# Performance work log

Measured on AMD Instinct MI355X. Metric: run time of the kernel, lower is better.

## Reference

```python
import jax, jax.numpy as jnp
import numpy as np
from jax import lax

B, ROWS, COLS, K, LATENT = 8, 1536, 16, 32, 16
EPS_REG = 0.01  # torchsort regularization_strength
BIG = 1e30


def setup_inputs() -> dict:
    key = jax.random.key(0)
    ks = jax.random.split(key, 12)
    def w(k, shape):
        return (jax.random.normal(k, shape, jnp.float32) / np.sqrt(shape[0])).astype(jnp.float32)
    return {
        "table": jax.random.uniform(ks[0], (B, ROWS, COLS), jnp.float32),
        "enc_w1": w(ks[1], (COLS, 32)), "enc_b1": 0.01 * jax.random.normal(ks[2], (32,), jnp.float32),
        "enc_w2": w(ks[3], (32, 64)),   "enc_b2": 0.01 * jax.random.normal(ks[4], (64,), jnp.float32),
        "mean_w": w(ks[5], (64, LATENT)), "mean_b": 0.01 * jax.random.normal(ks[6], (LATENT,), jnp.float32),
        "dec_w1": w(ks[7], (LATENT, 32)), "dec_b1": 0.01 * jax.random.normal(ks[8], (32,), jnp.float32),
        "dec_w2": w(ks[9], (32, COLS)),   "dec_b2": 0.01 * jax.random.normal(ks[10], (COLS,), jnp.float32),
        "labels": jax.random.randint(ks[11], (ROWS,), 0, K, jnp.int32),
        "BlockSize": 64,
        "current_epoch": 0,
        "baseline": 0,
    }


def _soft_rank_l2(s, eps):
    # Exact soft_rank (Blondel et al. / torchsort, l2 reg, ascending):
    # project s/eps onto permutahedron of (n,...,1).
    n = s.shape[0]
    x = s / eps
    perm = jnp.argsort(-x)            # descending sort
    xs = x[perm]
    w = jnp.arange(n, 0, -1, dtype=x.dtype)
    # dual = non-increasing isotonic fit of y = xs - w == -iso_inc(-(xs - w))
    y = -(xs - w)
    S = jnp.concatenate([jnp.zeros((1,), x.dtype), jnp.cumsum(y)])
    idx = jnp.arange(n)
    length = jnp.maximum(idx[None, :] - idx[:, None] + 1, 1).astype(x.dtype)
    A = (S[1:][None, :] - S[:n][:, None]) / length           # mean(y[j..k])  [j,k]
    A = jnp.where(idx[None, :] >= idx[:, None], A, BIG)
    Bm = lax.cummin(A, axis=1, reverse=True)                  # min_{k>=i} A[j,k]
    Cm = lax.cummax(Bm, axis=0)                               # max_{j<=i} ...
    iso_inc = jnp.diagonal(Cm)
    dual = -iso_inc
    primal = xs - dual
    inv = jnp.argsort(perm)
    return primal[inv]


def _forward(table, enc_w1, enc_b1, enc_w2, enc_b2, mean_w, mean_b,
             dec_w1, dec_b1, dec_w2, dec_b2, labels, BlockSize):
    b = table.shape[0]
    # VAE (autoencoder path; z = latent mean)
    h = jax.nn.relu(table @ enc_w1 + enc_b1)
    h = jax.nn.relu(h @ enc_w2 + enc_b2)
    z = h @ mean_w + mean_b                                   # [B, rows, 16]
    r = jax.nn.relu(z @ dec_w1 + dec_b1)
    recon = jax.nn.relu(r @ dec_w2 + dec_b2)
    loss = jnp.mean((recon - table) ** 2)
    # clustering scores (labels fixed from batch 0, shared across batch)
    onehot = jax.nn.one_hot(labels, K, dtype=z.dtype)         # [rows, K]
    counts = jnp.maximum(onehot.sum(0), 1.0)                  # [K]
    centers = jnp.einsum('brd,rk->bkd', z, onehot) / counts[None, :, None]
    center_data = centers[:, labels, :]                       # gather back [B, rows, 16]
    d2 = jnp.mean((z - center_data) ** 2, axis=-1)            # [B, rows]
    mn = d2.min(axis=1, keepdims=True); mx = d2.max(axis=1, keepdims=True)
    d2 = (d2 - mn) / (mx - mn)
    scores = d2 + labels.astype(z.dtype)[None, :]
    # training branch
    smn = scores.min(axis=1, keepdims=True); smx = scores.max(axis=1, keepdims=True)
    scaled = (scores - smn) / (smx - smn) * jnp.asarray(b, z.dtype)  # * len(table)
    ranks = jax.vmap(lambda s: _soft_rank_l2(s, EPS_REG))(scaled)
    rank_idx = jnp.argsort(jnp.argsort(scores, axis=1), axis=1) // BlockSize + 1
    rows = table.shape[1]
    return (ranks.reshape(b, rows, 1), rank_idx.reshape(b, rows, 1),
            scores.reshape(b, rows, 1), loss)


def reference(table, enc_w1, enc_b1, enc_w2, enc_b2, mean_w, mean_b,
              dec_w1, dec_b1, dec_w2, dec_b2, labels, BlockSize,
              current_epoch, baseline):
    return _forward(table, enc_w1, enc_b1, enc_w2, enc_b2, mean_w, mean_b,
                    dec_w1, dec_b1, dec_w2, dec_b2, labels, BlockSize)
```

## Files before the change

kernel.cpp:

```cpp
#include <hip/hip_runtime.h>

#define BATCH 8
#define ROWS 1536
#define KCLS 32
#define NTOT (BATCH*ROWS)
#define ELEMS (NTOT*16)
#define SSTRIDE 3073
#define BIGF 1.0e30f

enum : int {
  WS_Z     = 0,
  WS_X     = WS_Z + NTOT*16,
  WS_XS    = WS_X + NTOT,
  WS_S     = WS_XS + NTOT,
  WS_DESC  = WS_S + BATCH*SSTRIDE,
  WS_ASCP  = WS_DESC + NTOT,
  WS_DSCP  = WS_ASCP + 4*NTOT,
  WS_GPART = WS_DSCP + 4*NTOT,
  WS_LOSSP = WS_GPART + BATCH*96*512,
};
#define WS_CPART WS_GPART

#define LW1  0
#define LB1  512
#define LW2  544
#define LB2  2592
#define LMW  2656
#define LMB  3680
#define LDW1 3696
#define LDB1 4208
#define LDW2 4240
#define LDB2 4752
#define LTOT 4768

#define AX   0
#define AH1  16
#define AH2  48
#define AZ   112
#define AR1  128
#define AREC 144
#define ASTRIDE 164

#define RPB 16

template<int IN_BASE, int IN_N, int OUT_BASE, int OUT_PW, int OUT_TOT,
         int WOFF, int BOFF, bool RELU>
__device__ __forceinline__ void layerw(float* __restrict__ act,
                                       const float* __restrict__ wsh,
                                       int lrow, int fway)
{
  const int o0 = fway * OUT_PW;
  float acc[OUT_PW];
#pragma unroll
  for (int j = 0; j < OUT_PW; ++j) acc[j] = wsh[BOFF + o0 + j];

  const float4* arow = reinterpret_cast<const float4*>(&act[lrow*ASTRIDE + IN_BASE]);
#pragma unroll 2
  for (int i4 = 0; i4 < IN_N/4; ++i4) {
    float4 sv = arow[i4];
    float svx[4];
    svx[0] = sv.x; svx[1] = sv.y; svx[2] = sv.z; svx[3] = sv.w;
#pragma unroll
    for (int u = 0; u < 4; ++u) {
      const float s = svx[u];
      const float* wp = &wsh[WOFF + (i4*4 + u)*OUT_TOT + o0];
      if constexpr (OUT_PW == 1) {
        acc[0] = fmaf(s, wp[0], acc[0]);
      } else if constexpr (OUT_PW == 2) {
        float2 w = *reinterpret_cast<const float2*>(wp);
        acc[0] = fmaf(s, w.x, acc[0]);
        acc[1] = fmaf(s, w.y, acc[1]);
      } else {
#pragma unroll
        for (int q = 0; q < OUT_PW/4; ++q) {
          float4 w = reinterpret_cast<const float4*>(wp)[q];
          acc[q*4+0] = fmaf(s, w.x, acc[q*4+0]);
          acc[q*4+1] = fmaf(s, w.y, acc[q*4+1]);
          acc[q*4+2] = fmaf(s, w.z, acc[q*4+2]);
          acc[q*4+3] = fmaf(s, w.w, acc[q*4+3]);
        }
      }
    }
  }
  float* orow = &act[lrow*ASTRIDE + OUT_BASE + o0];
  if constexpr (OUT_PW == 1) {
    orow[0] = RELU ? fmaxf(acc[0], 0.f) : acc[0];
  } else if constexpr (OUT_PW == 2) {
    float2 v;
    v.x = RELU ? fmaxf(acc[0], 0.f) : acc[0];
    v.y = RELU ? fmaxf(acc[1], 0.f) : acc[1];
    *reinterpret_cast<float2*>(orow) = v;
  } else {
#pragma unroll
    for (int q = 0; q < OUT_PW/4; ++q) {
      float4 v;
      v.x = RELU ? fmaxf(acc[q*4+0], 0.f) : acc[q*4+0];
      v.y = RELU ? fmaxf(acc[q*4+1], 0.f) : acc[q*4+1];
      v.z = RELU ? fmaxf(acc[q*4+2], 0.f) : acc[q*4+2];
      v.w = RELU ? fmaxf(acc[q*4+3], 0.f) : acc[q*4+3];
      reinterpret_cast<float4*>(orow)[q] = v;
    }
  }
}

__global__ __launch_bounds__(256, 4) void k1_ae(
    const float* __restrict__ table,
    const float* __restrict__ w1, const float* __restrict__ b1,
    const float* __restrict__ w2, const float* __restrict__ b2,
    const float* __restrict__ mw, const float* __restrict__ mb,
    const float* __restrict__ dw1, const float* __restrict__ db1,
    const float* __restrict__ dw2, const float* __restrict__ db2,
    const int* __restrict__ labels,
    float* __restrict__ ws)
{
  const int tid  = threadIdx.x;
  const int lrow = tid & (RPB-1);
  const int fway = tid >> 4;
  const int blk  = blockIdx.x;
  const int b    = blk / 96;
  const int ch   = blk % 96;

  __shared__ float wsh[LTOT];
  __shared__ float act[RPB * ASTRIDE];
  __shared__ int   lbl[RPB];
  __shared__ float lred[4];

  {
    float4* d4 = reinterpret_cast<float4*>(wsh);
#define CPY(off, src, nf4) \
    { const float4* p = reinterpret_cast<const float4*>(src); \
      for (int t = tid; t < (nf4); t += 256) d4[(off)/4 + t] = p[t]; }
    CPY(LW1,  w1,  128) CPY(LB1,  b1,  8)  CPY(LW2,  w2,  512)
    CPY(LB2,  b2,  16)  CPY(LMW,  mw,  256) CPY(LMB,  mb,  4)
    CPY(LDW1, dw1, 128) CPY(LDB1, db1, 8)  CPY(LDW2, dw2, 128)
    CPY(LDB2, db2, 4)
#undef CPY
    if (tid < RPB) lbl[tid] = labels[ch * RPB + tid];
    if (tid < RPB*4) {
      const float4 v = reinterpret_cast<const float4*>(table)[blk*(RPB*4) + tid];
      reinterpret_cast<float4*>(act)[(tid >> 2)*(ASTRIDE/4) + (tid & 3)] = v;
    }
  }
  __syncthreads();

  layerw<AX,  16, AH1, 2, 32, LW1,  LB1,  true >(act, wsh, lrow, fway);
  __syncthreads();
  layerw<AH1, 32, AH2, 4, 64, LW2,  LB2,  true >(act, wsh, lrow, fway);
  __syncthreads();
  layerw<AH2, 64, AZ,  1, 16, LMW,  LMB,  false>(act, wsh, lrow, fway);
  __syncthreads();

  if (tid < RPB*4) {
    const float4 zv =
      reinterpret_cast<const float4*>(act)[(tid >> 2)*(ASTRIDE/4) + (AZ/4) + (tid & 3)];
    reinterpret_cast<float4*>(ws + WS_Z)[blk*(RPB*4) + tid] = zv;
  }

  layerw<AZ,  16, AR1, 2, 32, LDW1, LDB1, true >(act, wsh, lrow, fway);
  __syncthreads();
  layerw<AR1, 32, AREC,1, 16, LDW2, LDB2, true >(act, wsh, lrow, fway);
  __syncthreads();

  {
    const float d = act[lrow*ASTRIDE + AREC + fway] - act[lrow*ASTRIDE + AX + fway];
    float ls = d * d;
    for (int off = 32; off > 0; off >>= 1) ls += __shfl_down(ls, off);
    if ((tid & 63) == 0) lred[tid >> 6] = ls;
    __syncthreads();
    if (tid == 0) ws[WS_LOSSP + blk] = (lred[0] + lred[1]) + (lred[2] + lred[3]);
  }

  {
    float a0 = 0.f, a1 = 0.f;
    const int d0 = tid & 15, k0 = tid >> 4;
    const int k1c = k0 + 16;
#pragma unroll
    for (int rr = 0; rr < RPB; ++rr) {
      const int lb = lbl[rr];
      const float zv = act[rr*ASTRIDE + AZ + d0];
      a0 += (lb == k0)  ? zv : 0.f;
      a1 += (lb == k1c) ? zv : 0.f;
    }
    ws[WS_CPART + (b*96 + ch)*512 + tid]       = a0;
    ws[WS_CPART + (b*96 + ch)*512 + 256 + tid] = a1;
  }
}

__global__ __launch_bounds__(256) void kmid(const int* __restrict__ labels,
                                            float* __restrict__ ws,
                                            float* __restrict__ out)
{
  const int bi = blockIdx.x;
  const int jb = bi & 3, rb = (bi >> 2) % 6, b = bi / 24;
  const int tid = threadIdx.x;

  __shared__ int   cnt[KCLS];
  __shared__ int   lbl_l[ROWS];
  __shared__ float cent[512];
  alignas(16) __shared__ float s_l[ROWS];
  alignas(16) __shared__ float d2x[ROWS];
  __shared__ float rmn[256], rmx[256];

  if (tid < KCLS) cnt[tid] = 0;
  if (bi == 0) {
    rmn[tid] = ws[WS_LOSSP + tid] + ws[WS_LOSSP + 256 + tid] + ws[WS_LOSSP + 512 + tid];
  }
  __syncthreads();
#pragma unroll
  for (int c = 0; c < 6; ++c) {
    const int lb = labels[c*256 + tid];
    lbl_l[c*256 + tid] = lb;
    atomicAdd(&cnt[lb], 1);
  }
  if (bi == 0) {
    for (int off = 128; off > 0; off >>= 1) {
      __syncthreads();
      if (tid < off) rmn[tid] += rmn[tid + off];
    }
    if (tid == 0) out[3*NTOT] = rmn[0] / (float)ELEMS;
  }
  __syncthreads();

#pragma unroll
  for (int e = tid; e < 512; e += 256) {
    float s = 0.f;
    for (int c = 0; c < 96; ++c) s += ws[WS_CPART + (b*96 + c)*512 + e];
    const int cn = cnt[e >> 4] > 1 ? cnt[e >> 4] : 1;
    cent[e] = s / (float)cn;
  }
  __syncthreads();

  float tmn = 3.0e38f, tmx = -3.0e38f;
#pragma unroll
  for (int c = 0; c < 6; ++c) {
    const int r = c*256 + tid;
    const int lb = lbl_l[r];
    const float4* zp = reinterpret_cast<const float4*>(ws + WS_Z + (b*ROWS + r)*16);
    const float4* cp = reinterpret_cast<const float4*>(&cent[lb*16]);
    float s = 0.f;
#pragma unroll
    for (int q = 0; q < 4; ++q) {
      float4 zv = zp[q], cv = cp[q];
      float d0 = zv.x - cv.x, d1 = zv.y - cv.y, d2_ = zv.z - cv.z, d3 = zv.w - cv.w;
      s += d0*d0 + d1*d1 + d2_*d2_ + d3*d3;
    }
    const float dv = s / 16.f;
    d2x[r] = dv;
    tmn = fminf(tmn, dv); tmx = fmaxf(tmx, dv);
  }
  rmn[tid] = tmn; rmx[tid] = tmx;
  __syncthreads();
  for (int off = 128; off > 0; off >>= 1) {
    if (tid < off) {
      rmn[tid] = fminf(rmn[tid], rmn[tid + off]);
      rmx[tid] = fmaxf(rmx[tid], rmx[tid + off]);
    }
    __syncthreads();
  }
  const float mn = rmn[0], mx = rmx[0];
  __syncthreads();

  tmn = 3.0e38f; tmx = -3.0e38f;
#pragma unroll
  for (int c = 0; c < 6; ++c) {
    const int r = c*256 + tid;
    const float sc = (d2x[r] - mn) / (mx - mn) + (float)lbl_l[r];
    s_l[r] = sc;
    if (jb == 0 && c == rb) out[2*NTOT + b*ROWS + r] = sc;
    tmn = fminf(tmn, sc); tmx = fmaxf(tmx, sc);
  }
  rmn[tid] = tmn; rmx[tid] = tmx;
  __syncthreads();
  for (int off = 128; off > 0; off >>= 1) {
    if (tid < off) {
      rmn[tid] = fminf(rmn[tid], rmn[tid + off]);
      rmx[tid] = fmaxf(rmx[tid], rmx[tid + off]);
    }
    __syncthreads();
  }
  const float smn = rmn[0], smx = rmx[0];
  __syncthreads();

#pragma unroll
  for (int c = 0; c < 6; ++c) {
    const int r = c*256 + tid;
    const float scl = (s_l[r] - smn) / (smx - smn) * 8.0f;
    const float xv = scl / 0.01f;
    d2x[r] = xv;
    if (jb == 0 && c == rb) ws[WS_X + b*ROWS + r] = xv;
  }
  __syncthreads();

  const int r0 = rb*256 + tid;
  const float si = s_l[r0], xi = d2x[r0];
  int asc = 0, dsc = 0;
  const int j0 = jb*384;
  const float4* s4p = reinterpret_cast<const float4*>(&s_l[j0]);
  const float4* x4p = reinterpret_cast<const float4*>(&d2x[j0]);
#pragma unroll 4
  for (int kk = 0; kk < 96; ++kk) {
    const float4 s4 = s4p[kk];
    const float4 x4 = x4p[kk];
    const int j = j0 + kk*4;
    asc += (s4.x < si || (s4.x == si && j   < r0)) ? 1 : 0;
    asc += (s4.y < si || (s4.y == si && j+1 < r0)) ? 1 : 0;
    asc += (s4.z < si || (s4.z == si && j+2 < r0)) ? 1 : 0;
    asc += (s4.w < si || (s4.w == si && j+3 < r0)) ? 1 : 0;
    dsc += (x4.x > xi || (x4.x == xi && j   < r0)) ? 1 : 0;
    dsc += (x4.y > xi || (x4.y == xi && j+1 < r0)) ? 1 : 0;
    dsc += (x4.z > xi || (x4.z == xi && j+2 < r0)) ? 1 : 0;
    dsc += (x4.w > xi || (x4.w == xi && j+3 < r0)) ? 1 : 0;
  }
  int* wsi = reinterpret_cast<int*>(ws);
  wsi[WS_ASCP + jb*NTOT + b*ROWS + r0] = asc;
  wsi[WS_DSCP + jb*NTOT + b*ROWS + r0] = dsc;
}

__global__ __launch_bounds__(256) void k67(const int* __restrict__ bsp,
                                           float* __restrict__ ws,
                                           float* __restrict__ out)
{
  const int b = blockIdx.x, tid = threadIdx.x;
  const int lane = tid & 63, wav = tid >> 6;
  __shared__ float xs_l[ROWS];
  __shared__ float wtot[4];
  const int* wsi = reinterpret_cast<const int*>(ws);
  int* wsw = reinterpret_cast<int*>(ws);
  const int BS = *bsp;
#pragma unroll
  for (int c = 0; c < 6; ++c) {
    const int r = c*256 + tid;
    const int idx = b*ROWS + r;
    int asc = 0, dsc = 0;
#pragma unroll
    for (int jb = 0; jb < 4; ++jb) {
      asc += wsi[WS_ASCP + jb*NTOT + idx];
      dsc += wsi[WS_DSCP + jb*NTOT + idx];
    }
    out[NTOT + idx] = (float)(asc / BS + 1);
    wsw[WS_DESC + idx] = dsc;
    xs_l[dsc] = ws[WS_X + idx];
  }
  __syncthreads();
  const int base = tid * 6;
  float y[6], own = 0.f;
#pragma unroll
  for (int u = 0; u < 6; ++u) {
    ws[WS_XS + b*ROWS + base + u] = xs_l[base + u];
    y[u] = (float)(ROWS - (base + u)) - xs_l[base + u];
    own += y[u];
  }
  float v = own;
#pragma unroll
  for (int d = 1; d < 64; d <<= 1) {
    float o = __shfl_up(v, d);
    if (lane >= d) v += o;
  }
  if (lane == 63) wtot[wav] = v;
  __syncthreads();
  float wpre = 0.f;
  for (int w = 0; w < wav; ++w) wpre += wtot[w];
  float run = wpre + (v - own);
  float* S = ws + WS_S + b*SSTRIDE;
#pragma unroll
  for (int u = 0; u < 6; ++u) { S[base + u] = run; run += y[u]; }
  if (tid == 255) S[ROWS] = run;
#pragma unroll
  for (int u = 0; u < 6; ++u) S[ROWS + 1 + tid*6 + u] = BIGF;
}

__global__ __launch_bounds__(256) void k8a(float* __restrict__ ws)
{
  const int bi = blockIdx.x;
  const int c = bi & 7, ib = (bi >> 3) % 6, b = bi / 48;
  const int tid = threadIdx.x;
  __shared__ float Sseg[448];
  __shared__ float invl[192];
  const float* S = ws + WS_S + b*SSTRIDE;
  const int ibase = ib*256;
  const int segbase = ibase + c*192 + 1;
  Sseg[tid] = S[segbase + tid];
  if (tid < 192) {
    Sseg[256 + tid] = S[segbase + 256 + tid];
    invl[tid] = 1.0f / (float)(c*192 + tid + 1);
  }
  __syncthreads();
  const int i = ibase + tid;
  const float Si = S[i];
  float gm = 3.0e38f;
#pragma unroll 8
  for (int k = 0; k < 192; ++k)
    gm = fminf(gm, (Sseg[tid + k] - Si) * invl[k]);
  ws[WS_GPART + (b*8 + c)*ROWS + i] = gm;
}

__global__ __launch_bounds__(768) void k8b(float* __restrict__ ws,
                                           float* __restrict__ out)
{
  const int b = blockIdx.x, tid = threadIdx.x;
  const int lane = tid & 63, wav = tid >> 6;
  __shared__ float g[ROWS];
  __shared__ float wtot[12];
  for (int t = tid; t < ROWS; t += 768) {
    float gm = 3.0e38f;
#pragma unroll
    for (int c = 0; c < 8; ++c)
      gm = fminf(gm, ws[WS_GPART + (b*8 + c)*ROWS + t]);
    g[t] = gm;
  }
  __syncthreads();
  const float a = g[2*tid], cc = g[2*tid + 1];
  float v = fmaxf(a, cc);
#pragma unroll
  for (int d = 1; d < 64; d <<= 1) {
    float o = __shfl_up(v, d);
    if (lane >= d) v = fmaxf(v, o);
  }
  if (lane == 63) wtot[wav] = v;
  __syncthreads();
  float wpre = -3.0e38f;
  for (int w = 0; w < wav; ++w) wpre = fmaxf(wpre, wtot[w]);
  float lex = __shfl_up(v, 1);
  if (lane == 0) lex = -3.0e38f;
  const float excl = fmaxf(wpre, lex);
  const float i0 = fmaxf(excl, a);
  const float i1 = fmaxf(i0, cc);
  g[2*tid] = i0; g[2*tid + 1] = i1;
  __syncthreads();
  const float* xs = ws + WS_XS + b*ROWS;
  const int* desc = reinterpret_cast<const int*>(ws) + WS_DESC + b*ROWS;
  for (int t = tid; t < ROWS; t += 768) {
    const int dr = desc[t];
    out[b*ROWS + t] = xs[dr] + g[dr];
  }
}

extern "C" void kernel_launch(void* const* d_in, const int* in_sizes, int n_in,
                              void* d_out, int out_size, void* d_ws, size_t ws_size,
                              hipStream_t stream) {
  const float* table = (const float*)d_in[0];
  const float* w1  = (const float*)d_in[1];
  const float* b1  = (const float*)d_in[2];
  const float* w2  = (const float*)d_in[3];
  const float* b2  = (const float*)d_in[4];
  const float* mw  = (const float*)d_in[5];
  const float* mb  = (const float*)d_in[6];
  const float* dw1 = (const float*)d_in[7];
  const float* db1 = (const float*)d_in[8];
  const float* dw2 = (const float*)d_in[9];
  const float* db2 = (const float*)d_in[10];
  const int* labels = (const int*)d_in[11];
  const int* bsp    = (const int*)d_in[12];
  float* out = (float*)d_out;
  float* ws  = (float*)d_ws;

  k1_ae<<<768, 256, 0, stream>>>(table, w1, b1, w2, b2, mw, mb, dw1, db1, dw2, db2, labels, ws);
  kmid<<<192, 256, 0, stream>>>(labels, ws, out);
  k67<<<8, 256, 0, stream>>>(bsp, ws, out);
  k8a<<<384, 256, 0, stream>>>(ws);
  k8b<<<8, 768, 0, stream>>>(ws, out);
}
```

Baseline: 66.00 us.

## Split kmid into centroid/distance kernel and counting kernel to avoid redundant work

```diff
diff --git a/kernel.cpp b/kernel.cpp
--- a/kernel.cpp
+++ b/kernel.cpp
@@ -18,6 +18,8 @@
   WS_DSCP  = WS_ASCP + 4*NTOT,
   WS_GPART = WS_DSCP + 4*NTOT,
   WS_LOSSP = WS_GPART + BATCH*96*512,
+  WS_D2    = WS_LOSSP + 768,
+  WS_MM    = WS_D2 + NTOT,
 };
 #define WS_CPART WS_GPART
 
@@ -186,55 +188,42 @@
   }
 }
 
-__global__ __launch_bounds__(256) void kmid(const int* __restrict__ labels,
+__global__ __launch_bounds__(256) void kcd2(const int* __restrict__ labels,
                                             float* __restrict__ ws,
                                             float* __restrict__ out)
 {
   const int bi = blockIdx.x;
-  const int jb = bi & 3, rb = (bi >> 2) % 6, b = bi / 24;
+  const int b = bi / 6, ib = bi % 6;
   const int tid = threadIdx.x;
 
   __shared__ int   cnt[KCLS];
-  __shared__ int   lbl_l[ROWS];
+  __shared__ int   lbls[256];
   __shared__ float cent[512];
-  alignas(16) __shared__ float s_l[ROWS];
-  alignas(16) __shared__ float d2x[ROWS];
   __shared__ float rmn[256], rmx[256];
 
   if (tid < KCLS) cnt[tid] = 0;
-  if (bi == 0) {
-    rmn[tid] = ws[WS_LOSSP + tid] + ws[WS_LOSSP + 256 + tid] + ws[WS_LOSSP + 512 + tid];
-  }
   __syncthreads();
 #pragma unroll
   for (int c = 0; c < 6; ++c) {
     const int lb = labels[c*256 + tid];
-    lbl_l[c*256 + tid] = lb;
+    if (c == ib) lbls[tid] = lb;
     atomicAdd(&cnt[lb], 1);
-  }
-  if (bi == 0) {
-    for (int off = 128; off > 0; off >>= 1) {
-      __syncthreads();
-      if (tid < off) rmn[tid] += rmn[tid + off];
-    }
-    if (tid == 0) out[3*NTOT] = rmn[0] / (float)ELEMS;
   }
   __syncthreads();
 
 #pragma unroll
   for (int e = tid; e < 512; e += 256) {
     float s = 0.f;
+#pragma unroll 8
     for (int c = 0; c < 96; ++c) s += ws[WS_CPART + (b*96 + c)*512 + e];
     const int cn = cnt[e >> 4] > 1 ? cnt[e >> 4] : 1;
     cent[e] = s / (float)cn;
   }
   __syncthreads();
 
-  float tmn = 3.0e38f, tmx = -3.0e38f;
-#pragma unroll
-  for (int c = 0; c < 6; ++c) {
-    const int r = c*256 + tid;
-    const int lb = lbl_l[r];
+  const int r = ib*256 + tid;
+  {
+    const int lb = lbls[tid];
     const float4* zp = reinterpret_cast<const float4*>(ws + WS_Z + (b*ROWS + r)*16);
     const float4* cp = reinterpret_cast<const float4*>(&cent[lb*16]);
     float s = 0.f;
@@ -245,10 +234,9 @@
       s += d0*d0 + d1*d1 + d2_*d2_ + d3*d3;
     }
     const float dv = s / 16.f;
-    d2x[r] = dv;
-    tmn = fminf(tmn, dv); tmx = fmaxf(tmx, dv);
-  }
-  rmn[tid] = tmn; rmx[tid] = tmx;
+    ws[WS_D2 + b*ROWS + r] = dv;
+    rmn[tid] = dv; rmx[tid] = dv;
+  }
   __syncthreads();
   for (int off = 128; off > 0; off >>= 1) {
     if (tid < off) {
@@ -257,14 +245,47 @@
     }
     __syncthreads();
   }
-  const float mn = rmn[0], mx = rmx[0];
-  __syncthreads();
-
-  tmn = 3.0e38f; tmx = -3.0e38f;
+  if (tid == 0) {
+    ws[WS_MM + bi*2]     = rmn[0];
+    ws[WS_MM + bi*2 + 1] = rmx[0];
+  }
+
+  if (bi == 0) {
+    __syncthreads();
+    rmn[tid] = ws[WS_LOSSP + tid] + ws[WS_LOSSP + 256 + tid] + ws[WS_LOSSP + 512 + tid];
+    __syncthreads();
+    for (int off = 128; off > 0; off >>= 1) {
+      if (tid < off) rmn[tid] += rmn[tid + off];
+      __syncthreads();
+    }
+    if (tid == 0) out[3*NTOT] = rmn[0] / (float)ELEMS;
+  }
+}
+
+__global__ __launch_bounds__(256) void kcount(const int* __restrict__ labels,
+                                              float* __restrict__ ws,
+                                              float* __restrict__ out)
+{
+  const int bi = blockIdx.x;
+  const int jb = bi & 3, rb = (bi >> 2) % 6, b = bi / 24;
+  const int tid = threadIdx.x;
+
+  alignas(16) __shared__ float s_l[ROWS];
+  alignas(16) __shared__ float x_l[ROWS];
+  __shared__ float rmn[256], rmx[256];
+
+  float mn = 3.0e38f, mx = -3.0e38f;
+#pragma unroll
+  for (int c = 0; c < 6; ++c) {
+    mn = fminf(mn, ws[WS_MM + (b*6 + c)*2]);
+    mx = fmaxf(mx, ws[WS_MM + (b*6 + c)*2 + 1]);
+  }
+
+  float tmn = 3.0e38f, tmx = -3.0e38f;
 #pragma unroll
   for (int c = 0; c < 6; ++c) {
     const int r = c*256 + tid;
-    const float sc = (d2x[r] - mn) / (mx - mn) + (float)lbl_l[r];
+    const float sc = (ws[WS_D2 + b*ROWS + r] - mn) / (mx - mn) + (float)labels[r];
     s_l[r] = sc;
     if (jb == 0 && c == rb) out[2*NTOT + b*ROWS + r] = sc;
     tmn = fminf(tmn, sc); tmx = fmaxf(tmx, sc);
@@ -279,24 +300,23 @@
     __syncthreads();
   }
   const float smn = rmn[0], smx = rmx[0];
-  __syncthreads();
 
 #pragma unroll
   for (int c = 0; c < 6; ++c) {
     const int r = c*256 + tid;
     const float scl = (s_l[r] - smn) / (smx - smn) * 8.0f;
     const float xv = scl / 0.01f;
-    d2x[r] = xv;
+    x_l[r] = xv;
     if (jb == 0 && c == rb) ws[WS_X + b*ROWS + r] = xv;
   }
   __syncthreads();
 
   const int r0 = rb*256 + tid;
-  const float si = s_l[r0], xi = d2x[r0];
+  const float si = s_l[r0], xi = x_l[r0];
   int asc = 0, dsc = 0;
   const int j0 = jb*384;
   const float4* s4p = reinterpret_cast<const float4*>(&s_l[j0]);
-  const float4* x4p = reinterpret_cast<const float4*>(&d2x[j0]);
+  const float4* x4p = reinterpret_cast<const float4*>(&x_l[j0]);
 #pragma unroll 4
   for (int kk = 0; kk < 96; ++kk) {
     const float4 s4 = s4p[kk];
@@ -455,7 +475,8 @@
   float* ws  = (float*)d_ws;
 
   k1_ae<<<768, 256, 0, stream>>>(table, w1, b1, w2, b2, mw, mb, dw1, db1, dw2, db2, labels, ws);
-  kmid<<<192, 256, 0, stream>>>(labels, ws, out);
+  kcd2<<<48, 256, 0, stream>>>(labels, ws, out);
+  kcount<<<192, 256, 0, stream>>>(labels, ws, out);
   k67<<<8, 256, 0, stream>>>(bsp, ws, out);
   k8a<<<384, 256, 0, stream>>>(ws);
   k8b<<<8, 768, 0, stream>>>(ws, out);
```

After: 69.99 us. +6.0%, slower.
